# Kernel tuning notes

Measured on AMD Instinct MI355X. Metric: run time of the kernel, lower is better.

Reference implementation:

```python
import jax, jax.numpy as jnp
import numpy as np

N, E, DIN, DH, DOUT = 50000, 800000, 256, 128, 64


def setup_inputs() -> dict:
    key = jax.random.key(0)
    ks = jax.random.split(key, 12)
    return {
        "h": jax.random.normal(ks[0], (N, DIN), jnp.float32),
        "src": jax.random.randint(ks[1], (E,), 0, N, jnp.int32),
        "dst": jax.random.randint(ks[2], (E,), 0, N, jnp.int32),
        "W1": jax.random.normal(ks[3], (DIN, DH), jnp.float32) * (DIN ** -0.5),
        "al1": jax.random.normal(ks[4], (DH,), jnp.float32) * (DH ** -0.5),
        "ar1": jax.random.normal(ks[5], (DH,), jnp.float32) * (DH ** -0.5),
        "W2": jax.random.normal(ks[6], (DH, DH), jnp.float32) * (DH ** -0.5),
        "al2": jax.random.normal(ks[7], (DH,), jnp.float32) * (DH ** -0.5),
        "ar2": jax.random.normal(ks[8], (DH,), jnp.float32) * (DH ** -0.5),
        "W3": jax.random.normal(ks[9], (DH, DOUT), jnp.float32) * (DH ** -0.5),
        "al3": jax.random.normal(ks[10], (DOUT,), jnp.float32) * (DOUT ** -0.5),
        "ar3": jax.random.normal(ks[11], (DOUT,), jnp.float32) * (DOUT ** -0.5),
    }


def gat_layer(h, W, al, ar, src, dst):
    """DGL GATConv, 1 head, no bias: proj -> leaky_relu edge scores -> edge softmax over dst -> scatter-sum."""
    n = h.shape[0]
    f = h @ W                                   # [N, d]
    el = f @ al                                 # [N]
    er = f @ ar                                 # [N]
    e = jax.nn.leaky_relu(el[src] + er[dst], negative_slope=0.2)  # [E]
    m = jax.ops.segment_max(e, dst, num_segments=n)
    m = jnp.where(jnp.isfinite(m), m, 0.0)      # zero-in-degree nodes
    m = jax.lax.stop_gradient(m)
    ex = jnp.exp(e - m[dst])                    # [E]
    z = jax.ops.segment_sum(ex, dst, num_segments=n)
    a = ex / jnp.maximum(z, 1e-9)[dst]          # [E] softmax weights
    return jax.ops.segment_sum(a[:, None] * f[src], dst, num_segments=n)


def reference(h, src, dst, W1, al1, ar1, W2, al2, ar2, W3, al3, ar3):
    x = gat_layer(h, W1, al1, ar1, src, dst)
    x = jax.nn.relu(x)                          # dropout = identity (eval)
    x = gat_layer(x, W2, al2, ar2, src, dst)
    x = jax.nn.relu(x)
    x = gat_layer(x, W3, al3, ar3, src, dst)    # mean over 1 head = identity
    return jax.nn.log_softmax(x, axis=-1)
```

## Files before the change

### kernel.cpp

```cpp
#include <hip/hip_runtime.h>
#include <math.h>

#define DIN 256
#define DHID 128
#define DOUTC 64
#define EPB 2048

typedef __attribute__((ext_vector_type(8))) short short8;
typedef __attribute__((ext_vector_type(4))) float f32x4;

static __device__ __forceinline__ float wave_max(float v){
  #pragma unroll
  for (int o=1;o<64;o<<=1) v = fmaxf(v, __shfl_xor(v,o,64));
  return v;
}
static __device__ __forceinline__ float wave_sum(float v){
  #pragma unroll
  for (int o=1;o<64;o<<=1) v += __shfl_xor(v,o,64);
  return v;
}

static __device__ __forceinline__ unsigned short bf16_rne(float x){
  unsigned int u = __float_as_uint(x);
  return (unsigned short)((u + 0x7FFFu + ((u>>16)&1u)) >> 16);
}
static __device__ __forceinline__ float bf16_to_f32(unsigned short h){
  return __uint_as_float(((unsigned int)h)<<16);
}
static __device__ __forceinline__ float blo(unsigned int u){ return __uint_as_float(u<<16); }
static __device__ __forceinline__ float bhi(unsigned int u){ return __uint_as_float(u & 0xffff0000u); }

__global__ __launch_bounds__(256) void rs_hist(const int* __restrict__ dst,
    int* __restrict__ ghist, int E, int NB){
  __shared__ int h[256];
  const int t = threadIdx.x, blk = blockIdx.x;
  h[t] = 0; __syncthreads();
  const int base = blk*EPB;
  #pragma unroll
  for (int i=0;i<EPB/256;i++){
    int j = base + i*256 + t;
    if (j < E) atomicAdd(&h[dst[j]>>8], 1);
  }
  __syncthreads();
  ghist[t*NB + blk] = h[t];
}

__global__ __launch_bounds__(256) void rs_scan(int* __restrict__ ghist,
    int* __restrict__ btot, int NB){
  __shared__ int b[256];
  __shared__ int carry;
  const int hb = blockIdx.x, t = threadIdx.x;
  if (t==0) carry = 0;
  __syncthreads();
  for (int c0=0; c0<NB; c0+=256){
    int i = c0 + t;
    int v = (i<NB)? ghist[hb*NB+i] : 0;
    b[t] = v; __syncthreads();
    #pragma unroll
    for (int o=1;o<256;o<<=1){
      int x = (t>=o)? b[t-o] : 0;
      __syncthreads();
      b[t] += x;
      __syncthreads();
    }
    if (i<NB) ghist[hb*NB+i] = carry + b[t] - v;
    __syncthreads();
    if (t==255) carry += b[255];
    __syncthreads();
  }
  if (t==255) btot[hb] = carry;
}

__global__ __launch_bounds__(256) void rs_scan2(int* __restrict__ btot,
    int* __restrict__ offsets, int N, int E){
  __shared__ int b[256];
  const int t = threadIdx.x;
  int v = btot[t];
  b[t] = v; __syncthreads();
  #pragma unroll
  for (int o=1;o<256;o<<=1){
    int x = (t>=o)? b[t-o] : 0;
    __syncthreads();
    b[t] += x;
    __syncthreads();
  }
  btot[t] = b[t] - v;
  if (t==255){ btot[256] = E; offsets[N] = E; }
}

__global__ __launch_bounds__(256) void rs_scatter(const int* __restrict__ src,
    const int* __restrict__ dst, const int* __restrict__ ghist,
    const int* __restrict__ btot, uint2* __restrict__ ebuf, int E, int NB){
  __shared__ int cur[256];
  const int t = threadIdx.x, blk = blockIdx.x;
  cur[t] = ghist[t*NB + blk] + btot[t];
  __syncthreads();
  const int base = blk*EPB;
  #pragma unroll
  for (int i=0;i<EPB/256;i++){
    int j = base + i*256 + t;
    if (j < E){
      int d = dst[j];
      int pos = atomicAdd(&cur[d>>8], 1);
      ebuf[pos] = make_uint2((unsigned)src[j], (unsigned)d);
    }
  }
}

__global__ __launch_bounds__(256) void bucket_sort(const uint2* __restrict__ ebuf,
    const int* __restrict__ btot, int* __restrict__ offsets,
    int* __restrict__ srcs, int N){
  __shared__ int h[256];
  __shared__ int b[256];
  const int hb = blockIdx.x, t = threadIdx.x;
  const int b0 = btot[hb], b1 = btot[hb+1];
  h[t] = 0; __syncthreads();
  for (int j=b0+t; j<b1; j+=256) atomicAdd(&h[ebuf[j].y & 255u], 1);
  __syncthreads();
  int v = h[t];
  b[t] = v; __syncthreads();
  #pragma unroll
  for (int o=1;o<256;o<<=1){
    int x = (t>=o)? b[t-o] : 0;
    __syncthreads();
    b[t] += x;
    __syncthreads();
  }
  const int excl = b[t] - v;
  const int node = hb*256 + t;
  if (node < N) offsets[node] = b0 + excl;
  h[t] = excl;
  __syncthreads();
  for (int j=b0+t; j<b1; j+=256){
    uint2 e = ebuf[j];
    int pos = b0 + atomicAdd(&h[e.y & 255u], 1);
    srcs[pos] = (int)e.x;
  }
}

template<int K, int NC>
static __device__ __forceinline__ void pack_one(const float* __restrict__ W,
    unsigned short* __restrict__ Wp, int idx){
  constexpr int CT = NC/16;
  int l = idx & 63, t = idx >> 6;
  int ct = t % CT, kt = t / CT;
  int col = ct*16 + (l & 15);
  int k0 = kt*32 + (l >> 4)*8;
  unsigned short* dstp = Wp + (size_t)idx*8;
  #pragma unroll
  for (int j=0;j<8;j++)
    dstp[j] = bf16_rne(W[(size_t)(k0+j)*NC + col]);
}

__global__ __launch_bounds__(256) void pack_all(const float* __restrict__ W1,
    const float* __restrict__ W2, const float* __restrict__ W3,
    unsigned short* __restrict__ Wp1, unsigned short* __restrict__ Wp2,
    unsigned short* __restrict__ Wp3){
  constexpr int N1 = (DIN/32)*(DHID/16)*64;
  constexpr int N2 = (DHID/32)*(DHID/16)*64;
  constexpr int N3 = (DHID/32)*(DOUTC/16)*64;
  int idx = blockIdx.x*256 + threadIdx.x;
  if (idx < N1) pack_one<DIN,DHID>(W1, Wp1, idx);
  else if (idx < N1+N2) pack_one<DHID,DHID>(W2, Wp2, idx-N1);
  else if (idx < N1+N2+N3) pack_one<DHID,DOUTC>(W3, Wp3, idx-N1-N2);
}

template<int K, int NC, bool AF32>
__global__ __launch_bounds__(256) void gemm_v3(const void* __restrict__ Av,
    const unsigned short* __restrict__ Wp,
    const float* __restrict__ al, const float* __restrict__ ar,
    unsigned short* __restrict__ Fb, float* __restrict__ el, float* __restrict__ er, int nrows)
{
  constexpr int CT = NC/16, KT = K/32;
  constexpr int CHUNK_KT = (32/CT) < KT ? (32/CT) : KT;
  constexpr int NCHUNK = KT / CHUNK_KT;
  constexpr int CHUNK_SHORTS = CHUNK_KT*CT*64*8;
  __shared__ unsigned short bsm[CHUNK_SHORTS];

  const float* Af = (const float*)Av;
  const unsigned short* Abf = (const unsigned short*)Av;

  const int tid = threadIdx.x;
  const int lane = tid & 63;
  const int wid  = tid >> 6;
  const int row0 = blockIdx.x*64 + wid*16;
  const int c = lane & 15, g = lane >> 4;
  const int arow = row0 + c;
  const bool aok = arow < nrows;

  f32x4 acc[CT];
  #pragma unroll
  for (int i=0;i<CT;i++) acc[i] = (f32x4)0.f;

  for (int ch=0; ch<NCHUNK; ++ch){
    if (ch) __syncthreads();
    {
      const uint4* gsrc = (const uint4*)Wp + (size_t)ch*(CHUNK_SHORTS/8);
      uint4* ldst = (uint4*)bsm;
      #pragma unroll
      for (int i=0; i<CHUNK_SHORTS/8/256; ++i)
        ldst[i*256 + tid] = gsrc[i*256 + tid];
    }
    __syncthreads();

    #pragma unroll
    for (int ktl=0; ktl<CHUNK_KT; ++ktl){
      const int k0 = (ch*CHUNK_KT + ktl)*32 + g*8;
      short8 ahi, alo;
      if constexpr (AF32){
        float xs[8];
        if (aok){
          float4 v0 = *(const float4*)&Af[(size_t)arow*K + k0];
          float4 v1 = *(const float4*)&Af[(size_t)arow*K + k0 + 4];
          xs[0]=v0.x; xs[1]=v0.y; xs[2]=v0.z; xs[3]=v0.w;
          xs[4]=v1.x; xs[5]=v1.y; xs[6]=v1.z; xs[7]=v1.w;
        } else {
          #pragma unroll
          for (int j=0;j<8;j++) xs[j]=0.f;
        }
        #pragma unroll
        for (int j=0;j<8;j++){
          unsigned short hh = bf16_rne(xs[j]);
          ahi[j] = (short)hh;
          alo[j] = (short)bf16_rne(xs[j] - bf16_to_f32(hh));
        }
      } else {
        if (aok) ahi = *(const short8*)&Abf[(size_t)arow*K + k0];
        else     ahi = (short8)0;
        alo = ahi;
      }
      #pragma unroll
      for (int ct=0; ct<CT; ++ct){
        short8 b = *(const short8*)&bsm[(ktl*CT+ct)*512 + lane*8];
        acc[ct] = __builtin_amdgcn_mfma_f32_16x16x32_bf16(ahi, b, acc[ct], 0,0,0);
        if constexpr (AF32)
          acc[ct] = __builtin_amdgcn_mfma_f32_16x16x32_bf16(alo, b, acc[ct], 0,0,0);
      }
    }
  }

  float alv[CT], arv[CT];
  #pragma unroll
  for (int ct=0;ct<CT;ct++){ alv[ct]=al[ct*16+c]; arv[ct]=ar[ct*16+c]; }
  #pragma unroll
  for (int j=0;j<4;j++){
    const int row = row0 + g*4 + j;
    const bool ok = row < nrows;
    float sl=0.f, sr=0.f;
    #pragma unroll
    for (int ct=0;ct<CT;ct++){
      float f = acc[ct][j];
      sl = fmaf(f, alv[ct], sl);
      sr = fmaf(f, arv[ct], sr);
      if (ok) Fb[(size_t)row*NC + ct*16 + c] = bf16_rne(f);
    }
    #pragma unroll
    for (int o=1;o<16;o<<=1){ sl += __shfl_xor(sl,o,64); sr += __shfl_xor(sr,o,64); }
    if (ok && c==0){ el[row]=sl; er[row]=sr; }
  }
}

template<int D, bool RELU, bool LOGSM, bool OUTBF>
__global__ __launch_bounds__(256) void agg4_kernel(const unsigned short* __restrict__ Fb,
    const float* __restrict__ el, const float* __restrict__ er,
    const int* __restrict__ offsets, const int* __restrict__ srcs,
    void* __restrict__ outv, int N)
{
  constexpr int CPL = D/16;
  __shared__ float2 ws[4][64];
  const int wv = threadIdx.x >> 6;
  const int lane = threadIdx.x & 63;
  const int c16 = lane & 15, g = lane >> 4;
  const int v = blockIdx.x*4 + wv;
  if (v >= N) return;
  const int o0 = offsets[v], o1 = offsets[v+1];
  const float erv = er[v];

  float m = -INFINITY, z = 0.f;
  float acc[CPL];
  #pragma unroll
  for (int i=0;i<CPL;i++) acc[i]=0.f;

  for (int s0 = o0; s0 < o1; s0 += 64){
    const int j = s0 + lane;
    int sidx = 0; float e = -INFINITY;
    if (j < o1){
      sidx = srcs[j];
      float tv = el[sidx] + erv;
      e = (tv > 0.f) ? tv : 0.2f*tv;
    }
    const float nm = fmaxf(m, wave_max(e));
    const float scale = __expf(m - nm);
    const float wgt = __expf(e - nm);
    z = z*scale + wave_sum(wgt);
    #pragma unroll
    for (int i=0;i<CPL;i++) acc[i] *= scale;
    m = nm;
    ws[wv][lane] = make_float2(wgt, __int_as_float(sidx));
    __builtin_amdgcn_wave_barrier();

    const int cnt = min(64, o1 - s0);
    int t = g;
    if constexpr (D == 128){
      for (; t+12 < cnt; t += 16){
        float2 p0 = ws[wv][t],   p1 = ws[wv][t+4];
        float2 p2 = ws[wv][t+8], p3 = ws[wv][t+12];
        uint4 u0 = *((const uint4*)(Fb + (size_t)__float_as_int(p0.y)*128) + c16);
        uint4 u1 = *((const uint4*)(Fb + (size_t)__float_as_int(p1.y)*128) + c16);
        uint4 u2 = *((const uint4*)(Fb + (size_t)__float_as_int(p2.y)*128) + c16);
        uint4 u3 = *((const uint4*)(Fb + (size_t)__float_as_int(p3.y)*128) + c16);
        acc[0]=fmaf(p0.x, blo(u0.x), acc[0]); acc[1]=fmaf(p0.x, bhi(u0.x), acc[1]);
        acc[2]=fmaf(p0.x, blo(u0.y), acc[2]); acc[3]=fmaf(p0.x, bhi(u0.y), acc[3]);
        acc[4]=fmaf(p0.x, blo(u0.z), acc[4]); acc[5]=fmaf(p0.x, bhi(u0.z), acc[5]);
        acc[6]=fmaf(p0.x, blo(u0.w), acc[6]); acc[7]=fmaf(p0.x, bhi(u0.w), acc[7]);
        acc[0]=fmaf(p1.x, blo(u1.x), acc[0]); acc[1]=fmaf(p1.x, bhi(u1.x), acc[1]);
        acc[2]=fmaf(p1.x, blo(u1.y), acc[2]); acc[3]=fmaf(p1.x, bhi(u1.y), acc[3]);
        acc[4]=fmaf(p1.x, blo(u1.z), acc[4]); acc[5]=fmaf(p1.x, bhi(u1.z), acc[5]);
        acc[6]=fmaf(p1.x, blo(u1.w), acc[6]); acc[7]=fmaf(p1.x, bhi(u1.w), acc[7]);
        acc[0]=fmaf(p2.x, blo(u2.x), acc[0]); acc[1]=fmaf(p2.x, bhi(u2.x), acc[1]);
        acc[2]=fmaf(p2.x, blo(u2.y), acc[2]); acc[3]=fmaf(p2.x, bhi(u2.y), acc[3]);
        acc[4]=fmaf(p2.x, blo(u2.z), acc[4]); acc[5]=fmaf(p2.x, bhi(u2.z), acc[5]);
        acc[6]=fmaf(p2.x, blo(u2.w), acc[6]); acc[7]=fmaf(p2.x, bhi(u2.w), acc[7]);
        acc[0]=fmaf(p3.x, blo(u3.x), acc[0]); acc[1]=fmaf(p3.x, bhi(u3.x), acc[1]);
        acc[2]=fmaf(p3.x, blo(u3.y), acc[2]); acc[3]=fmaf(p3.x, bhi(u3.y), acc[3]);
        acc[4]=fmaf(p3.x, blo(u3.z), acc[4]); acc[5]=fmaf(p3.x, bhi(u3.z), acc[5]);
        acc[6]=fmaf(p3.x, blo(u3.w), acc[6]); acc[7]=fmaf(p3.x, bhi(u3.w), acc[7]);
      }
      for (; t < cnt; t += 4){
        float2 p0 = ws[wv][t];
        uint4 u0 = *((const uint4*)(Fb + (size_t)__float_as_int(p0.y)*128) + c16);
        acc[0]=fmaf(p0.x, blo(u0.x), acc[0]); acc[1]=fmaf(p0.x, bhi(u0.x), acc[1]);
        acc[2]=fmaf(p0.x, blo(u0.y), acc[2]); acc[3]=fmaf(p0.x, bhi(u0.y), acc[3]);
        acc[4]=fmaf(p0.x, blo(u0.z), acc[4]); acc[5]=fmaf(p0.x, bhi(u0.z), acc[5]);
        acc[6]=fmaf(p0.x, blo(u0.w), acc[6]); acc[7]=fmaf(p0.x, bhi(u0.w), acc[7]);
      }
    } else {
      for (; t+12 < cnt; t += 16){
        float2 p0 = ws[wv][t],   p1 = ws[wv][t+4];
        float2 p2 = ws[wv][t+8], p3 = ws[wv][t+12];
        uint2 u0 = *((const uint2*)(Fb + (size_t)__float_as_int(p0.y)*64) + c16);
        uint2 u1 = *((const uint2*)(Fb + (size_t)__float_as_int(p1.y)*64) + c16);
        uint2 u2 = *((const uint2*)(Fb + (size_t)__float_as_int(p2.y)*64) + c16);
        uint2 u3 = *((const uint2*)(Fb + (size_t)__float_as_int(p3.y)*64) + c16);
        acc[0]=fmaf(p0.x, blo(u0.x), acc[0]); acc[1]=fmaf(p0.x, bhi(u0.x), acc[1]);
        acc[2]=fmaf(p0.x, blo(u0.y), acc[2]); acc[3]=fmaf(p0.x, bhi(u0.y), acc[3]);
        acc[0]=fmaf(p1.x, blo(u1.x), acc[0]); acc[1]=fmaf(p1.x, bhi(u1.x), acc[1]);
        acc[2]=fmaf(p1.x, blo(u1.y), acc[2]); acc[3]=fmaf(p1.x, bhi(u1.y), acc[3]);
        acc[0]=fmaf(p2.x, blo(u2.x), acc[0]); acc[1]=fmaf(p2.x, bhi(u2.x), acc[1]);
        acc[2]=fmaf(p2.x, blo(u2.y), acc[2]); acc[3]=fmaf(p2.x, bhi(u2.y), acc[3]);
        acc[0]=fmaf(p3.x, blo(u3.x), acc[0]); acc[1]=fmaf(p3.x, bhi(u3.x), acc[1]);
        acc[2]=fmaf(p3.x, blo(u3.y), acc[2]); acc[3]=fmaf(p3.x, bhi(u3.y), acc[3]);
      }
      for (; t < cnt; t += 4){
        float2 p0 = ws[wv][t];
        uint2 u0 = *((const uint2*)(Fb + (size_t)__float_as_int(p0.y)*64) + c16);
        acc[0]=fmaf(p0.x, blo(u0.x), acc[0]); acc[1]=fmaf(p0.x, bhi(u0.x), acc[1]);
        acc[2]=fmaf(p0.x, blo(u0.y), acc[2]); acc[3]=fmaf(p0.x, bhi(u0.y), acc[3]);
      }
    }
    __builtin_amdgcn_wave_barrier();
  }

  #pragma unroll
  for (int i=0;i<CPL;i++){
    acc[i] += __shfl_xor(acc[i],16,64);
    acc[i] += __shfl_xor(acc[i],32,64);
  }
  const float zi = 1.f / fmaxf(z, 1e-9f);

  if constexpr (LOGSM){
    float* out = (float*)outv;
    float y[CPL];
    #pragma unroll
    for (int i=0;i<CPL;i++) y[i] = acc[i]*zi;
    float M = y[0];
    #pragma unroll
    for (int i=1;i<CPL;i++) M = fmaxf(M, y[i]);
    #pragma unroll
    for (int o=1;o<16;o<<=1) M = fmaxf(M, __shfl_xor(M,o,64));
    float ssum = 0.f;
    #pragma unroll
    for (int i=0;i<CPL;i++) ssum += __expf(y[i]-M);
    #pragma unroll
    for (int o=1;o<16;o<<=1) ssum += __shfl_xor(ssum,o,64);
    const float lw = M + logf(ssum);
    if (g==0){
      float4 r = make_float4(y[0]-lw, y[1]-lw, y[2]-lw, y[3]-lw);
      *(float4*)&out[(size_t)v*64 + c16*4] = r;
    }
  } else if constexpr (OUTBF){
    unsigned short* outb = (unsigned short*)outv;
    if (g==0){
      short8 o8;
      #pragma unroll
      for (int i=0;i<CPL;i++){
        float r = acc[i]*zi;
        if (RELU) r = fmaxf(r,0.f);
        o8[i] = (short)bf16_rne(r);
      }
      *(short8*)&outb[(size_t)v*128 + c16*8] = o8;
    }
  }
}

extern "C" void kernel_launch(void* const* d_in, const int* in_sizes, int n_in,
                              void* d_out, int out_size, void* d_ws, size_t ws_size,
                              hipStream_t stream) {
  const float* h   = (const float*)d_in[0];
  const int*   src = (const int*)d_in[1];
  const int*   dst = (const int*)d_in[2];
  const float* W1  = (const float*)d_in[3];
  const float* al1 = (const float*)d_in[4];
  const float* ar1 = (const float*)d_in[5];
  const float* W2  = (const float*)d_in[6];
  const float* al2 = (const float*)d_in[7];
  const float* ar2 = (const float*)d_in[8];
  const float* W3  = (const float*)d_in[9];
  const float* al3 = (const float*)d_in[10];
  const float* ar3 = (const float*)d_in[11];

  const int N = in_sizes[0] / DIN;
  const int E = in_sizes[1];
  const int NB = (E + EPB - 1) / EPB;
  const int NHB = (N + 255) / 256;

  auto alignup = [](size_t x){ return (x + 255) & ~(size_t)255; };
  char* p = (char*)d_ws;
  int* offsets = (int*)p; p += alignup(((size_t)N+1)*4);
  int* srcs    = (int*)p; p += alignup((size_t)E*4);
  int* ghist   = (int*)p; p += alignup((size_t)256*NB*4);
  int* btot    = (int*)p; p += alignup(257*4);
  uint2* ebuf  = (uint2*)p; p += alignup((size_t)E*8);
  unsigned short* Fb = (unsigned short*)p; p += alignup((size_t)N*DHID*2);
  unsigned short* X  = (unsigned short*)p; p += alignup((size_t)N*DHID*2);
  float* el    = (float*)p; p += alignup((size_t)N*4);
  float* er    = (float*)p; p += alignup((size_t)N*4);
  unsigned short* Wp1 = (unsigned short*)p; p += alignup((size_t)(DIN/32)*(DHID/16)*64*8*2);
  unsigned short* Wp2 = (unsigned short*)p; p += alignup((size_t)(DHID/32)*(DHID/16)*64*8*2);
  unsigned short* Wp3 = (unsigned short*)p; p += alignup((size_t)(DHID/32)*(DOUTC/16)*64*8*2);

  const int nbW4 = (N+3)/4;
  const int nbG  = (N+63)/64;

  pack_all<<<28,256,0,stream>>>(W1, W2, W3, Wp1, Wp2, Wp3);

  rs_hist   <<<NB, 256,0,stream>>>(dst, ghist, E, NB);
  rs_scan   <<<256,256,0,stream>>>(ghist, btot, NB);
  rs_scan2  <<<1,  256,0,stream>>>(btot, offsets, N, E);
  rs_scatter<<<NB, 256,0,stream>>>(src, dst, ghist, btot, ebuf, E, NB);
  bucket_sort<<<NHB,256,0,stream>>>(ebuf, btot, offsets, srcs, N);

  gemm_v3<DIN,DHID,true><<<nbG,256,0,stream>>>(h, Wp1, al1, ar1, Fb, el, er, N);
  agg4_kernel<128,true,false,true><<<nbW4,256,0,stream>>>(Fb, el, er, offsets, srcs, X, N);

  gemm_v3<DHID,DHID,false><<<nbG,256,0,stream>>>(X, Wp2, al2, ar2, Fb, el, er, N);
  agg4_kernel<128,true,false,true><<<nbW4,256,0,stream>>>(Fb, el, er, offsets, srcs, X, N);

  gemm_v3<DHID,DOUTC,false><<<nbG,256,0,stream>>>(X, Wp3, al3, ar3, Fb, el, er, N);
  agg4_kernel<64,false,true,false><<<nbW4,256,0,stream>>>(Fb, el, er, offsets, srcs, d_out, N);
}
```

Baseline: 185.7 us.

## Split 128-wide aggregation across two column-half blocks and pack edge buffer

The aggregation kernel now handles 64 columns per wave, and the 128-wide layers launch a second grid dimension so each half of the feature columns is gathered by a separate block. Each wave loads 8-byte gathers instead of 16-byte ones, which raises parallelism and lowers register use. The cost is that the edge-score softmax work (el gather, max, exp, sum) is done twice. The radix-sort scatter buffer also packs src<<8 | (dst&255) into one 32-bit word instead of a uint2, halving that buffer's traffic. This packing assumes src fits in 24 bits.

```diff
diff --git a/kernel.cpp b/kernel.cpp
--- a/kernel.cpp
+++ b/kernel.cpp
@@ -90,7 +90,7 @@
 
 __global__ __launch_bounds__(256) void rs_scatter(const int* __restrict__ src,
     const int* __restrict__ dst, const int* __restrict__ ghist,
-    const int* __restrict__ btot, uint2* __restrict__ ebuf, int E, int NB){
+    const int* __restrict__ btot, unsigned int* __restrict__ ebuf, int E, int NB){
   __shared__ int cur[256];
   const int t = threadIdx.x, blk = blockIdx.x;
   cur[t] = ghist[t*NB + blk] + btot[t];
@@ -102,12 +102,12 @@
     if (j < E){
       int d = dst[j];
       int pos = atomicAdd(&cur[d>>8], 1);
-      ebuf[pos] = make_uint2((unsigned)src[j], (unsigned)d);
-    }
-  }
-}
-
-__global__ __launch_bounds__(256) void bucket_sort(const uint2* __restrict__ ebuf,
+      ebuf[pos] = ((unsigned)src[j] << 8) | ((unsigned)d & 255u);
+    }
+  }
+}
+
+__global__ __launch_bounds__(256) void bucket_sort(const unsigned int* __restrict__ ebuf,
     const int* __restrict__ btot, int* __restrict__ offsets,
     int* __restrict__ srcs, int N){
   __shared__ int h[256];
@@ -115,7 +115,7 @@
   const int hb = blockIdx.x, t = threadIdx.x;
   const int b0 = btot[hb], b1 = btot[hb+1];
   h[t] = 0; __syncthreads();
-  for (int j=b0+t; j<b1; j+=256) atomicAdd(&h[ebuf[j].y & 255u], 1);
+  for (int j=b0+t; j<b1; j+=256) atomicAdd(&h[ebuf[j] & 255u], 1);
   __syncthreads();
   int v = h[t];
   b[t] = v; __syncthreads();
@@ -132,9 +132,9 @@
   h[t] = excl;
   __syncthreads();
   for (int j=b0+t; j<b1; j+=256){
-    uint2 e = ebuf[j];
-    int pos = b0 + atomicAdd(&h[e.y & 255u], 1);
-    srcs[pos] = (int)e.x;
+    unsigned int e = ebuf[j];
+    int pos = b0 + atomicAdd(&h[e & 255u], 1);
+    srcs[pos] = (int)(e >> 8);
   }
 }
 
@@ -261,25 +261,23 @@
 }
 
 template<int D, bool RELU, bool LOGSM, bool OUTBF>
-__global__ __launch_bounds__(256) void agg4_kernel(const unsigned short* __restrict__ Fb,
+__global__ __launch_bounds__(256) void agg5_kernel(const unsigned short* __restrict__ Fb,
     const float* __restrict__ el, const float* __restrict__ er,
     const int* __restrict__ offsets, const int* __restrict__ srcs,
     void* __restrict__ outv, int N)
 {
-  constexpr int CPL = D/16;
   __shared__ float2 ws[4][64];
   const int wv = threadIdx.x >> 6;
   const int lane = threadIdx.x & 63;
   const int c16 = lane & 15, g = lane >> 4;
   const int v = blockIdx.x*4 + wv;
   if (v >= N) return;
+  const int colbase = blockIdx.y * 64;
   const int o0 = offsets[v], o1 = offsets[v+1];
   const float erv = er[v];
 
   float m = -INFINITY, z = 0.f;
-  float acc[CPL];
-  #pragma unroll
-  for (int i=0;i<CPL;i++) acc[i]=0.f;
+  float acc[4] = {0.f,0.f,0.f,0.f};
 
   for (int s0 = o0; s0 < o1; s0 += 64){
     const int j = s0 + lane;
@@ -294,75 +292,40 @@
     const float wgt = __expf(e - nm);
     z = z*scale + wave_sum(wgt);
     #pragma unroll
-    for (int i=0;i<CPL;i++) acc[i] *= scale;
+    for (int i=0;i<4;i++) acc[i] *= scale;
     m = nm;
     ws[wv][lane] = make_float2(wgt, __int_as_float(sidx));
     __builtin_amdgcn_wave_barrier();
 
     const int cnt = min(64, o1 - s0);
     int t = g;
-    if constexpr (D == 128){
-      for (; t+12 < cnt; t += 16){
-        float2 p0 = ws[wv][t],   p1 = ws[wv][t+4];
-        float2 p2 = ws[wv][t+8], p3 = ws[wv][t+12];
-        uint4 u0 = *((const uint4*)(Fb + (size_t)__float_as_int(p0.y)*128) + c16);
-        uint4 u1 = *((const uint4*)(Fb + (size_t)__float_as_int(p1.y)*128) + c16);
-        uint4 u2 = *((const uint4*)(Fb + (size_t)__float_as_int(p2.y)*128) + c16);
-        uint4 u3 = *((const uint4*)(Fb + (size_t)__float_as_int(p3.y)*128) + c16);
-        acc[0]=fmaf(p0.x, blo(u0.x), acc[0]); acc[1]=fmaf(p0.x, bhi(u0.x), acc[1]);
-        acc[2]=fmaf(p0.x, blo(u0.y), acc[2]); acc[3]=fmaf(p0.x, bhi(u0.y), acc[3]);
-        acc[4]=fmaf(p0.x, blo(u0.z), acc[4]); acc[5]=fmaf(p0.x, bhi(u0.z), acc[5]);
-        acc[6]=fmaf(p0.x, blo(u0.w), acc[6]); acc[7]=fmaf(p0.x, bhi(u0.w), acc[7]);
-        acc[0]=fmaf(p1.x, blo(u1.x), acc[0]); acc[1]=fmaf(p1.x, bhi(u1.x), acc[1]);
-        acc[2]=fmaf(p1.x, blo(u1.y), acc[2]); acc[3]=fmaf(p1.x, bhi(u1.y), acc[3]);
-        acc[4]=fmaf(p1.x, blo(u1.z), acc[4]); acc[5]=fmaf(p1.x, bhi(u1.z), acc[5]);
-        acc[6]=fmaf(p1.x, blo(u1.w), acc[6]); acc[7]=fmaf(p1.x, bhi(u1.w), acc[7]);
-        acc[0]=fmaf(p2.x, blo(u2.x), acc[0]); acc[1]=fmaf(p2.x, bhi(u2.x), acc[1]);
-        acc[2]=fmaf(p2.x, blo(u2.y), acc[2]); acc[3]=fmaf(p2.x, bhi(u2.y), acc[3]);
-        acc[4]=fmaf(p2.x, blo(u2.z), acc[4]); acc[5]=fmaf(p2.x, bhi(u2.z), acc[5]);
-        acc[6]=fmaf(p2.x, blo(u2.w), acc[6]); acc[7]=fmaf(p2.x, bhi(u2.w), acc[7]);
-        acc[0]=fmaf(p3.x, blo(u3.x), acc[0]); acc[1]=fmaf(p3.x, bhi(u3.x), acc[1]);
-        acc[2]=fmaf(p3.x, blo(u3.y), acc[2]); acc[3]=fmaf(p3.x, bhi(u3.y), acc[3]);
-        acc[4]=fmaf(p3.x, blo(u3.z), acc[4]); acc[5]=fmaf(p3.x, bhi(u3.z), acc[5]);
-        acc[6]=fmaf(p3.x, blo(u3.w), acc[6]); acc[7]=fmaf(p3.x, bhi(u3.w), acc[7]);
-      }
-      for (; t < cnt; t += 4){
-        float2 p0 = ws[wv][t];
-        uint4 u0 = *((const uint4*)(Fb + (size_t)__float_as_int(p0.y)*128) + c16);
-        acc[0]=fmaf(p0.x, blo(u0.x), acc[0]); acc[1]=fmaf(p0.x, bhi(u0.x), acc[1]);
-        acc[2]=fmaf(p0.x, blo(u0.y), acc[2]); acc[3]=fmaf(p0.x, bhi(u0.y), acc[3]);
-        acc[4]=fmaf(p0.x, blo(u0.z), acc[4]); acc[5]=fmaf(p0.x, bhi(u0.z), acc[5]);
-        acc[6]=fmaf(p0.x, blo(u0.w), acc[6]); acc[7]=fmaf(p0.x, bhi(u0.w), acc[7]);
-      }
-    } else {
-      for (; t+12 < cnt; t += 16){
-        float2 p0 = ws[wv][t],   p1 = ws[wv][t+4];
-        float2 p2 = ws[wv][t+8], p3 = ws[wv][t+12];
-        uint2 u0 = *((const uint2*)(Fb + (size_t)__float_as_int(p0.y)*64) + c16);
-        uint2 u1 = *((const uint2*)(Fb + (size_t)__float_as_int(p1.y)*64) + c16);
-        uint2 u2 = *((const uint2*)(Fb + (size_t)__float_as_int(p2.y)*64) + c16);
-        uint2 u3 = *((const uint2*)(Fb + (size_t)__float_as_int(p3.y)*64) + c16);
-        acc[0]=fmaf(p0.x, blo(u0.x), acc[0]); acc[1]=fmaf(p0.x, bhi(u0.x), acc[1]);
-        acc[2]=fmaf(p0.x, blo(u0.y), acc[2]); acc[3]=fmaf(p0.x, bhi(u0.y), acc[3]);
-        acc[0]=fmaf(p1.x, blo(u1.x), acc[0]); acc[1]=fmaf(p1.x, bhi(u1.x), acc[1]);
-        acc[2]=fmaf(p1.x, blo(u1.y), acc[2]); acc[3]=fmaf(p1.x, bhi(u1.y), acc[3]);
-        acc[0]=fmaf(p2.x, blo(u2.x), acc[0]); acc[1]=fmaf(p2.x, bhi(u2.x), acc[1]);
-        acc[2]=fmaf(p2.x, blo(u2.y), acc[2]); acc[3]=fmaf(p2.x, bhi(u2.y), acc[3]);
-        acc[0]=fmaf(p3.x, blo(u3.x), acc[0]); acc[1]=fmaf(p3.x, bhi(u3.x), acc[1]);
-        acc[2]=fmaf(p3.x, blo(u3.y), acc[2]); acc[3]=fmaf(p3.x, bhi(u3.y), acc[3]);
-      }
-      for (; t < cnt; t += 4){
-        float2 p0 = ws[wv][t];
-        uint2 u0 = *((const uint2*)(Fb + (size_t)__float_as_int(p0.y)*64) + c16);
-        acc[0]=fmaf(p0.x, blo(u0.x), acc[0]); acc[1]=fmaf(p0.x, bhi(u0.x), acc[1]);
-        acc[2]=fmaf(p0.x, blo(u0.y), acc[2]); acc[3]=fmaf(p0.x, bhi(u0.y), acc[3]);
-      }
+    for (; t+12 < cnt; t += 16){
+      float2 p0 = ws[wv][t],   p1 = ws[wv][t+4];
+      float2 p2 = ws[wv][t+8], p3 = ws[wv][t+12];
+      uint2 u0 = *((const uint2*)(Fb + (size_t)__float_as_int(p0.y)*D + colbase) + c16);
+      uint2 u1 = *((const uint2*)(Fb + (size_t)__float_as_int(p1.y)*D + colbase) + c16);
+      uint2 u2 = *((const uint2*)(Fb + (size_t)__float_as_int(p2.y)*D + colbase) + c16);
+      uint2 u3 = *((const uint2*)(Fb + (size_t)__float_as_int(p3.y)*D + colbase) + c16);
+      acc[0]=fmaf(p0.x, blo(u0.x), acc[0]); acc[1]=fmaf(p0.x, bhi(u0.x), acc[1]);
+      acc[2]=fmaf(p0.x, blo(u0.y), acc[2]); acc[3]=fmaf(p0.x, bhi(u0.y), acc[3]);
+      acc[0]=fmaf(p1.x, blo(u1.x), acc[0]); acc[1]=fmaf(p1.x, bhi(u1.x), acc[1]);
+      acc[2]=fmaf(p1.x, blo(u1.y), acc[2]); acc[3]=fmaf(p1.x, bhi(u1.y), acc[3]);
+      acc[0]=fmaf(p2.x, blo(u2.x), acc[0]); acc[1]=fmaf(p2.x, bhi(u2.x), acc[1]);
+      acc[2]=fmaf(p2.x, blo(u2.y), acc[2]); acc[3]=fmaf(p2.x, bhi(u2.y), acc[3]);
+      acc[0]=fmaf(p3.x, blo(u3.x), acc[0]); acc[1]=fmaf(p3.x, bhi(u3.x), acc[1]);
+      acc[2]=fmaf(p3.x, blo(u3.y), acc[2]); acc[3]=fmaf(p3.x, bhi(u3.y), acc[3]);
+    }
+    for (; t < cnt; t += 4){
+      float2 p0 = ws[wv][t];
+      uint2 u0 = *((const uint2*)(Fb + (size_t)__float_as_int(p0.y)*D + colbase) + c16);
+      acc[0]=fmaf(p0.x, blo(u0.x), acc[0]); acc[1]=fmaf(p0.x, bhi(u0.x), acc[1]);
+      acc[2]=fmaf(p0.x, blo(u0.y), acc[2]); acc[3]=fmaf(p0.x, bhi(u0.y), acc[3]);
     }
     __builtin_amdgcn_wave_barrier();
   }
 
   #pragma unroll
-  for (int i=0;i<CPL;i++){
+  for (int i=0;i<4;i++){
     acc[i] += __shfl_xor(acc[i],16,64);
     acc[i] += __shfl_xor(acc[i],32,64);
   }
@@ -370,17 +333,15 @@
 
   if constexpr (LOGSM){
     float* out = (float*)outv;
-    float y[CPL];
-    #pragma unroll
-    for (int i=0;i<CPL;i++) y[i] = acc[i]*zi;
-    float M = y[0];
-    #pragma unroll
-    for (int i=1;i<CPL;i++) M = fmaxf(M, y[i]);
+    float y[4];
+    #pragma unroll
+    for (int i=0;i<4;i++) y[i] = acc[i]*zi;
+    float M = fmaxf(fmaxf(y[0],y[1]), fmaxf(y[2],y[3]));
     #pragma unroll
     for (int o=1;o<16;o<<=1) M = fmaxf(M, __shfl_xor(M,o,64));
     float ssum = 0.f;
     #pragma unroll
-    for (int i=0;i<CPL;i++) ssum += __expf(y[i]-M);
+    for (int i=0;i<4;i++) ssum += __expf(y[i]-M);
     #pragma unroll
     for (int o=1;o<16;o<<=1) ssum += __shfl_xor(ssum,o,64);
     const float lw = M + logf(ssum);
@@ -391,14 +352,14 @@
   } else if constexpr (OUTBF){
     unsigned short* outb = (unsigned short*)outv;
     if (g==0){
-      short8 o8;
-      #pragma unroll
-      for (int i=0;i<CPL;i++){
-        float r = acc[i]*zi;
-        if (RELU) r = fmaxf(r,0.f);
-        o8[i] = (short)bf16_rne(r);
-      }
-      *(short8*)&outb[(size_t)v*128 + c16*8] = o8;
+      unsigned int b0, b1, b2, b3;
+      float r0 = acc[0]*zi, r1 = acc[1]*zi, r2 = acc[2]*zi, r3 = acc[3]*zi;
+      if (RELU){ r0=fmaxf(r0,0.f); r1=fmaxf(r1,0.f); r2=fmaxf(r2,0.f); r3=fmaxf(r3,0.f); }
+      b0 = bf16_rne(r0); b1 = bf16_rne(r1); b2 = bf16_rne(r2); b3 = bf16_rne(r3);
+      uint2 o;
+      o.x = b0 | (b1<<16);
+      o.y = b2 | (b3<<16);
+      *(uint2*)&outb[(size_t)v*D + colbase + c16*4] = o;
     }
   }
 }
@@ -430,7 +391,7 @@
   int* srcs    = (int*)p; p += alignup((size_t)E*4);
   int* ghist   = (int*)p; p += alignup((size_t)256*NB*4);
   int* btot    = (int*)p; p += alignup(257*4);
-  uint2* ebuf  = (uint2*)p; p += alignup((size_t)E*8);
+  unsigned int* ebuf = (unsigned int*)p; p += alignup((size_t)E*4);
   unsigned short* Fb = (unsigned short*)p; p += alignup((size_t)N*DHID*2);
   unsigned short* X  = (unsigned short*)p; p += alignup((size_t)N*DHID*2);
   float* el    = (float*)p; p += alignup((size_t)N*4);
@@ -451,11 +412,11 @@
   bucket_sort<<<NHB,256,0,stream>>>(ebuf, btot, offsets, srcs, N);
 
   gemm_v3<DIN,DHID,true><<<nbG,256,0,stream>>>(h, Wp1, al1, ar1, Fb, el, er, N);
-  agg4_kernel<128,true,false,true><<<nbW4,256,0,stream>>>(Fb, el, er, offsets, srcs, X, N);
+  agg5_kernel<128,true,false,true><<<dim3(nbW4,2),256,0,stream>>>(Fb, el, er, offsets, srcs, X, N);
 
   gemm_v3<DHID,DHID,false><<<nbG,256,0,stream>>>(X, Wp2, al2, ar2, Fb, el, er, N);
-  agg4_kernel<128,true,false,true><<<nbW4,256,0,stream>>>(Fb, el, er, offsets, srcs, X, N);
+  agg5_kernel<128,true,false,true><<<dim3(nbW4,2),256,0,stream>>>(Fb, el, er, offsets, srcs, X, N);
 
   gemm_v3<DHID,DOUTC,false><<<nbG,256,0,stream>>>(X, Wp3, al3, ar3, Fb, el, er, N);
-  agg4_kernel<64,false,true,false><<<nbW4,256,0,stream>>>(Fb, el, er, offsets, srcs, d_out, N);
-}
+  agg5_kernel<64,false,true,false><<<dim3(nbW4,1),256,0,stream>>>(Fb, el, er, offsets, srcs, d_out, N);
+}
```

Measured after the change: 204.8 us. 10.3% more time.

## Precompute per-edge softmax weights in a separate kernel and pack sort keys

Applied to the files above, without the earlier changes.

Splits the edge softmax out of the aggregation kernel. A new thread-per-node kernel computes the max, the normalised weights and writes them to a per-edge buffer, so the aggregation wave only reads weights and sources and no longer runs the online rescaling with wave reductions. The radix-sort scratch is also packed from uint2 to a single 32-bit word (src<<8 | low dst bits), halving its traffic. The cost is an extra launch per layer, one thread per node looping serially over its edges three times (load imbalance), and an extra E-sized write and read.

```diff
diff --git a/kernel.cpp b/kernel.cpp
--- a/kernel.cpp
+++ b/kernel.cpp
@@ -8,17 +8,6 @@
 
 typedef __attribute__((ext_vector_type(8))) short short8;
 typedef __attribute__((ext_vector_type(4))) float f32x4;
-
-static __device__ __forceinline__ float wave_max(float v){
-  #pragma unroll
-  for (int o=1;o<64;o<<=1) v = fmaxf(v, __shfl_xor(v,o,64));
-  return v;
-}
-static __device__ __forceinline__ float wave_sum(float v){
-  #pragma unroll
-  for (int o=1;o<64;o<<=1) v += __shfl_xor(v,o,64);
-  return v;
-}
 
 static __device__ __forceinline__ unsigned short bf16_rne(float x){
   unsigned int u = __float_as_uint(x);
@@ -90,7 +79,7 @@
 
 __global__ __launch_bounds__(256) void rs_scatter(const int* __restrict__ src,
     const int* __restrict__ dst, const int* __restrict__ ghist,
-    const int* __restrict__ btot, uint2* __restrict__ ebuf, int E, int NB){
+    const int* __restrict__ btot, unsigned int* __restrict__ ebuf, int E, int NB){
   __shared__ int cur[256];
   const int t = threadIdx.x, blk = blockIdx.x;
   cur[t] = ghist[t*NB + blk] + btot[t];
@@ -102,12 +91,12 @@
     if (j < E){
       int d = dst[j];
       int pos = atomicAdd(&cur[d>>8], 1);
-      ebuf[pos] = make_uint2((unsigned)src[j], (unsigned)d);
-    }
-  }
-}
-
-__global__ __launch_bounds__(256) void bucket_sort(const uint2* __restrict__ ebuf,
+      ebuf[pos] = ((unsigned)src[j] << 8) | ((unsigned)d & 255u);
+    }
+  }
+}
+
+__global__ __launch_bounds__(256) void bucket_sort(const unsigned int* __restrict__ ebuf,
     const int* __restrict__ btot, int* __restrict__ offsets,
     int* __restrict__ srcs, int N){
   __shared__ int h[256];
@@ -115,7 +104,7 @@
   const int hb = blockIdx.x, t = threadIdx.x;
   const int b0 = btot[hb], b1 = btot[hb+1];
   h[t] = 0; __syncthreads();
-  for (int j=b0+t; j<b1; j+=256) atomicAdd(&h[ebuf[j].y & 255u], 1);
+  for (int j=b0+t; j<b1; j+=256) atomicAdd(&h[ebuf[j] & 255u], 1);
   __syncthreads();
   int v = h[t];
   b[t] = v; __syncthreads();
@@ -132,9 +121,9 @@
   h[t] = excl;
   __syncthreads();
   for (int j=b0+t; j<b1; j+=256){
-    uint2 e = ebuf[j];
-    int pos = b0 + atomicAdd(&h[e.y & 255u], 1);
-    srcs[pos] = (int)e.x;
+    unsigned int e = ebuf[j];
+    int pos = b0 + atomicAdd(&h[e & 255u], 1);
+    srcs[pos] = (int)(e >> 8);
   }
 }
 
@@ -260,9 +249,35 @@
   }
 }
 
+__global__ __launch_bounds__(256) void stats_w(const float* __restrict__ el,
+    const float* __restrict__ er, const int* __restrict__ offsets,
+    const int* __restrict__ srcs, float* __restrict__ w, int N){
+  const int v = blockIdx.x*256 + threadIdx.x;
+  if (v >= N) return;
+  const int o0 = offsets[v], o1 = offsets[v+1];
+  if (o0 == o1) return;
+  const float erv = er[v];
+  float m = -INFINITY;
+  for (int j=o0; j<o1; ++j){
+    float t = el[srcs[j]] + erv;
+    t = (t > 0.f) ? t : 0.2f*t;
+    m = fmaxf(m, t);
+  }
+  float z = 0.f;
+  for (int j=o0; j<o1; ++j){
+    float t = el[srcs[j]] + erv;
+    t = (t > 0.f) ? t : 0.2f*t;
+    float e = __expf(t - m);
+    z += e;
+    w[j] = e;
+  }
+  const float zi = 1.f / fmaxf(z, 1e-9f);
+  for (int j=o0; j<o1; ++j) w[j] *= zi;
+}
+
 template<int D, bool RELU, bool LOGSM, bool OUTBF>
-__global__ __launch_bounds__(256) void agg4_kernel(const unsigned short* __restrict__ Fb,
-    const float* __restrict__ el, const float* __restrict__ er,
+__global__ __launch_bounds__(256) void agg6_kernel(const unsigned short* __restrict__ Fb,
+    const float* __restrict__ w,
     const int* __restrict__ offsets, const int* __restrict__ srcs,
     void* __restrict__ outv, int N)
 {
@@ -274,29 +289,14 @@
   const int v = blockIdx.x*4 + wv;
   if (v >= N) return;
   const int o0 = offsets[v], o1 = offsets[v+1];
-  const float erv = er[v];
-
-  float m = -INFINITY, z = 0.f;
+
   float acc[CPL];
   #pragma unroll
   for (int i=0;i<CPL;i++) acc[i]=0.f;
 
   for (int s0 = o0; s0 < o1; s0 += 64){
     const int j = s0 + lane;
-    int sidx = 0; float e = -INFINITY;
-    if (j < o1){
-      sidx = srcs[j];
-      float tv = el[sidx] + erv;
-      e = (tv > 0.f) ? tv : 0.2f*tv;
-    }
-    const float nm = fmaxf(m, wave_max(e));
-    const float scale = __expf(m - nm);
-    const float wgt = __expf(e - nm);
-    z = z*scale + wave_sum(wgt);
-    #pragma unroll
-    for (int i=0;i<CPL;i++) acc[i] *= scale;
-    m = nm;
-    ws[wv][lane] = make_float2(wgt, __int_as_float(sidx));
+    if (j < o1) ws[wv][lane] = make_float2(w[j], __int_as_float(srcs[j]));
     __builtin_amdgcn_wave_barrier();
 
     const int cnt = min(64, o1 - s0);
@@ -366,26 +366,22 @@
     acc[i] += __shfl_xor(acc[i],16,64);
     acc[i] += __shfl_xor(acc[i],32,64);
   }
-  const float zi = 1.f / fmaxf(z, 1e-9f);
 
   if constexpr (LOGSM){
     float* out = (float*)outv;
-    float y[CPL];
-    #pragma unroll
-    for (int i=0;i<CPL;i++) y[i] = acc[i]*zi;
-    float M = y[0];
-    #pragma unroll
-    for (int i=1;i<CPL;i++) M = fmaxf(M, y[i]);
+    float M = acc[0];
+    #pragma unroll
+    for (int i=1;i<CPL;i++) M = fmaxf(M, acc[i]);
     #pragma unroll
     for (int o=1;o<16;o<<=1) M = fmaxf(M, __shfl_xor(M,o,64));
     float ssum = 0.f;
     #pragma unroll
-    for (int i=0;i<CPL;i++) ssum += __expf(y[i]-M);
+    for (int i=0;i<CPL;i++) ssum += __expf(acc[i]-M);
     #pragma unroll
     for (int o=1;o<16;o<<=1) ssum += __shfl_xor(ssum,o,64);
     const float lw = M + logf(ssum);
     if (g==0){
-      float4 r = make_float4(y[0]-lw, y[1]-lw, y[2]-lw, y[3]-lw);
+      float4 r = make_float4(acc[0]-lw, acc[1]-lw, acc[2]-lw, acc[3]-lw);
       *(float4*)&out[(size_t)v*64 + c16*4] = r;
     }
   } else if constexpr (OUTBF){
@@ -394,7 +390,7 @@
       short8 o8;
       #pragma unroll
       for (int i=0;i<CPL;i++){
-        float r = acc[i]*zi;
+        float r = acc[i];
         if (RELU) r = fmaxf(r,0.f);
         o8[i] = (short)bf16_rne(r);
       }
@@ -428,9 +424,10 @@
   char* p = (char*)d_ws;
   int* offsets = (int*)p; p += alignup(((size_t)N+1)*4);
   int* srcs    = (int*)p; p += alignup((size_t)E*4);
+  float* wbuf  = (float*)p; p += alignup((size_t)E*4);
   int* ghist   = (int*)p; p += alignup((size_t)256*NB*4);
   int* btot    = (int*)p; p += alignup(257*4);
-  uint2* ebuf  = (uint2*)p; p += alignup((size_t)E*8);
+  unsigned int* ebuf = (unsigned int*)p; p += alignup((size_t)E*4);
   unsigned short* Fb = (unsigned short*)p; p += alignup((size_t)N*DHID*2);
   unsigned short* X  = (unsigned short*)p; p += alignup((size_t)N*DHID*2);
   float* el    = (float*)p; p += alignup((size_t)N*4);
@@ -440,6 +437,7 @@
   unsigned short* Wp3 = (unsigned short*)p; p += alignup((size_t)(DHID/32)*(DOUTC/16)*64*8*2);
 
   const int nbW4 = (N+3)/4;
+  const int nbN  = (N+255)/256;
   const int nbG  = (N+63)/64;
 
   pack_all<<<28,256,0,stream>>>(W1, W2, W3, Wp1, Wp2, Wp3);
@@ -451,11 +449,14 @@
   bucket_sort<<<NHB,256,0,stream>>>(ebuf, btot, offsets, srcs, N);
 
   gemm_v3<DIN,DHID,true><<<nbG,256,0,stream>>>(h, Wp1, al1, ar1, Fb, el, er, N);
-  agg4_kernel<128,true,false,true><<<nbW4,256,0,stream>>>(Fb, el, er, offsets, srcs, X, N);
+  stats_w<<<nbN,256,0,stream>>>(el, er, offsets, srcs, wbuf, N);
+  agg6_kernel<128,true,false,true><<<nbW4,256,0,stream>>>(Fb, wbuf, offsets, srcs, X, N);
 
   gemm_v3<DHID,DHID,false><<<nbG,256,0,stream>>>(X, Wp2, al2, ar2, Fb, el, er, N);
-  agg4_kernel<128,true,false,true><<<nbW4,256,0,stream>>>(Fb, el, er, offsets, srcs, X, N);
+  stats_w<<<nbN,256,0,stream>>>(el, er, offsets, srcs, wbuf, N);
+  agg6_kernel<128,true,false,true><<<nbW4,256,0,stream>>>(Fb, wbuf, offsets, srcs, X, N);
 
   gemm_v3<DHID,DOUTC,false><<<nbG,256,0,stream>>>(X, Wp3, al3, ar3, Fb, el, er, N);
-  agg4_kernel<64,false,true,false><<<nbW4,256,0,stream>>>(Fb, el, er, offsets, srcs, d_out, N);
-}
+  stats_w<<<nbN,256,0,stream>>>(el, er, offsets, srcs, wbuf, N);
+  agg6_kernel<64,false,true,false><<<nbW4,256,0,stream>>>(Fb, wbuf, offsets, srcs, d_out, N);
+}
```

New measurement: 234.1 us. 1.26x slower.
